# Performance work log

Measured on AMD Instinct MI355X. Metric: run time of the kernel, lower is better.

Reference implementation:

```python
import jax, jax.numpy as jnp
import numpy as np

EMBED_DIM = 512
PATCH = 16
QUANT_N = 1024
QUANT_DIM = 256
LN_EPS = 1e-5


def setup_inputs() -> dict:
    key = jax.random.key(0)
    k1, k2, k3, k4 = jax.random.split(key, 4)
    B, T, M = 16, 8192, 128
    fbank = jax.random.normal(k1, (B, T, M), dtype=jnp.float32)
    # xavier-normal conv weight (O,I,kH,kW), frozen in the original module
    fan = PATCH * PATCH + EMBED_DIM
    conv_w = jax.random.normal(k2, (EMBED_DIM, 1, PATCH, PATCH), dtype=jnp.float32) * np.sqrt(2.0 / fan)
    proj = jax.random.normal(k3, (EMBED_DIM, QUANT_DIM), dtype=jnp.float32) * np.sqrt(2.0 / (EMBED_DIM + QUANT_DIM))
    codebook = jax.random.normal(k4, (QUANT_N, QUANT_DIM), dtype=jnp.float32)
    return {"fbank": fbank, "conv_w": conv_w, "proj": proj, "codebook": codebook}


def _l2norm(x, eps=1e-12):
    return x / jnp.maximum(jnp.linalg.norm(x, axis=-1, keepdims=True), eps)


def reference(fbank, conv_w, proj, codebook):
    # patch embedding: Conv2d(1, D, k=16, s=16) over (B, 1, T, mel)
    x = fbank[:, None, :, :]  # B,1,T,M
    feats = jax.lax.conv_general_dilated(
        x, conv_w, window_strides=(PATCH, PATCH), padding='VALID',
        dimension_numbers=('NCHW', 'OIHW', 'NCHW'))  # B,D,T/16,M/16
    B, D, H, W = feats.shape
    feats = feats.reshape(B, D, H * W).transpose(0, 2, 1)  # B,N,D
    # LayerNorm without affine
    mu = jnp.mean(feats, axis=-1, keepdims=True)
    var = jnp.var(feats, axis=-1, keepdims=True)
    feats = (feats - mu) * jax.lax.rsqrt(var + LN_EPS)
    # random projection quantizer: l2norm(x @ P) vs l2-normalized codebook;
    # argmin euclidean distance == argmax cosine similarity for unit vectors
    p = _l2norm(jnp.einsum('bnd,dq->bnq', feats, proj))  # B,N,Q
    cb = _l2norm(codebook)                                # K,Q
    sim = jnp.einsum('bnq,kq->bnk', p, cb)                # B,N,K
    embed_ind = jnp.argmax(sim, axis=-1)                  # B,N int
    return embed_ind
```

## Files before the change

kernel.cpp:

```cpp
#include <hip/hip_runtime.h>
#include <math.h>

#define QD 256
#define QN 1024
#define TT 8192

typedef __bf16 bf16x8 __attribute__((ext_vector_type(8)));
typedef float  f32x16 __attribute__((ext_vector_type(16)));
typedef unsigned short ushort_t;
typedef unsigned short us8 __attribute__((ext_vector_type(8)));

#define PL  0
#define WS_ 49152
#define P1_ 50176
#define MU_ 51200
#define LM_ 53248
#define TN_ 53376
#define LX_ 54400
#define TH_ 55424
#define CN_ 55552
#define CC_ 55680
#define SMEM_TOTAL 59776

__device__ __forceinline__ void split3(float x, ushort_t& h, ushort_t& m, ushort_t& l) {
    unsigned int xu = __float_as_uint(x);
    h = (ushort_t)(xu >> 16);
    float hf = __uint_as_float(xu & 0xFFFF0000u);
    float r1 = x - hf;
    unsigned int r1u = __float_as_uint(r1);
    m = (ushort_t)(r1u >> 16);
    float mf = __uint_as_float(r1u & 0xFFFF0000u);
    float r2 = r1 - mf;
    l = (ushort_t)(__float_as_uint(r2) >> 16);
}
__device__ __forceinline__ f32x16 MF(bf16x8 a, bf16x8 b, f32x16 c) {
    return __builtin_amdgcn_mfma_f32_32x32x16_bf16(a, b, c, 0, 0, 0);
}

__global__ __launch_bounds__(256) void k_pre(const float* __restrict__ convw,
                                             const float* __restrict__ proj,
                                             const float* __restrict__ cb,
                                             ushort_t* __restrict__ cbph,
                                             float* __restrict__ cbn,
                                             ushort_t* __restrict__ w2p,
                                             float* __restrict__ wsum,
                                             float* __restrict__ p1) {
    int bx = blockIdx.x, t = threadIdx.x;
    if (bx < 256) {
        int c = bx*4 + (t>>6), lane = t&63;
        float4 v = ((const float4*)(cb + (size_t)c*QD))[lane];
        float ss = v.x*v.x + v.y*v.y + v.z*v.z + v.w*v.w;
        #pragma unroll
        for (int off = 32; off > 0; off >>= 1) ss += __shfl_down(ss, off);
        ss = __shfl(ss, 0);
        float inv = 1.0f/fmaxf(sqrtf(ss), 1e-12f);
        float4 vn = make_float4(v.x*inv, v.y*inv, v.z*inv, v.w*inv);
        *(float4*)(cbn + (size_t)c*QD + 4*lane) = vn;
        float vals[4] = {vn.x, vn.y, vn.z, vn.w};
        #pragma unroll
        for (int i = 0; i < 4; ++i) {
            int k = 4*lane + i;
            size_t base = ((size_t)(k>>4)*32 + (c>>5))*512 + (((k>>3)&1)*32 + (c&31))*8 + (k&7);
            cbph[base] = (ushort_t)(__float_as_uint(vals[i]) >> 16);
        }
    } else if (bx < 320) {
        int col0 = (bx - 256) * 4;
        __shared__ float4 colv4[512];
        const float* src = proj + col0;
        colv4[t]       = *(const float4*)(src + (size_t)t * 256);
        colv4[t + 256] = *(const float4*)(src + (size_t)(t + 256) * 256);
        __syncthreads();
        float a0 = 0.f, a1 = 0.f, a2 = 0.f, a3 = 0.f;
        #pragma unroll 16
        for (int d = 0; d < 512; ++d) {
            float wv = convw[d*256 + t];
            float4 cv = colv4[d];
            a0 += wv*cv.x; a1 += wv*cv.y; a2 += wv*cv.z; a3 += wv*cv.w;
        }
        float accs[4] = {a0, a1, a2, a3};
        #pragma unroll
        for (int j = 0; j < 4; ++j) {
            int col = col0 + j;
            ushort_t hb, mb, lb; split3(accs[j], hb, mb, lb);
            size_t base = ((size_t)(t>>4)*8 + (col>>5))*512 + (((t>>3)&1)*32 + (col&31))*8 + (t&7);
            w2p[base] = hb;
            w2p[base + 65536] = mb;
            w2p[base + 131072] = lb;
        }
    } else if (bx == 320) {
        float s = 0.f;
        #pragma unroll 32
        for (int d = 0; d < 512; ++d) s += convw[d*256 + t];
        wsum[t] = s;
    } else {
        float s = 0.f;
        #pragma unroll 32
        for (int d = 0; d < 512; ++d) s += proj[d*256 + t];
        p1[t] = s;
    }
}

__global__ __launch_bounds__(512, 4) void k_mega(const float* __restrict__ fbank,
                                                 const ushort_t* __restrict__ w2p,
                                                 const ushort_t* __restrict__ cbph,
                                                 const float* __restrict__ cbn,
                                                 const float* __restrict__ wsum,
                                                 const float* __restrict__ p1,
                                                 int* __restrict__ out) {
    __shared__ char smem[SMEM_TOTAL];
    float* wsS   = (float*)(smem + WS_);
    float* p1S   = (float*)(smem + P1_);
    float* muS   = (float*)(smem + MU_);
    float* lnMuS = (float*)(smem + LM_);
    float* tn2P  = (float*)(smem + TN_);
    float* lmaxS = (float*)(smem + LX_);
    float* thrS  = (float*)(smem + TH_);
    int*   cntS  = (int*)(smem + CN_);
    ushort_t* candS = (ushort_t*)(smem + CC_);

    int tid = threadIdx.x;
    int n0 = blockIdx.x * 32;
    int w = tid >> 6, lane = tid & 63;
    int n31 = lane & 31, h = lane >> 5;
    size_t loff = (size_t)lane * 16;
    const char* w2pc = (const char*)w2p;
    const char* cbhc = (const char*)cbph;

    auto loadB1 = [&](int kcv, bf16x8 (&dst)[3]) {
        #pragma unroll
        for (int q = 0; q < 3; ++q)
            dst[q] = *(const bf16x8*)(w2pc + (size_t)q*131072 + (size_t)(kcv*8 + w)*1024 + loff);
    };
    auto loadB2 = [&](int kcv, bf16x8 (&dst)[4]) {
        dst[0] = *(const bf16x8*)(cbhc + (size_t)(kcv*32 + w     )*1024 + loff);
        dst[1] = *(const bf16x8*)(cbhc + (size_t)(kcv*32 + w + 8 )*1024 + loff);
        dst[2] = *(const bf16x8*)(cbhc + (size_t)(kcv*32 + w + 16)*1024 + loff);
        dst[3] = *(const bf16x8*)(cbhc + (size_t)(kcv*32 + w + 24)*1024 + loff);
    };
    auto loadA = [&](int kcv, bf16x8 (&a)[3]) {
        #pragma unroll
        for (int p = 0; p < 3; ++p)
            a[p] = *(const bf16x8*)(smem + p*16384 + kcv*1024 + loff);
    };
    auto compute6 = [&](bf16x8 (&a)[3], bf16x8 (&b)[3], f32x16& acc) {
        acc = MF(a[0], b[0], acc);
        acc = MF(a[0], b[1], acc);
        acc = MF(a[1], b[0], acc);
        acc = MF(a[1], b[1], acc);
        acc = MF(a[0], b[2], acc);
        acc = MF(a[2], b[0], acc);
    };

    float4 va[2], vb[2];
    #pragma unroll
    for (int i = 0; i < 2; ++i) {
        int id = tid + 512*i;
        int kc = id >> 6, cl = id & 63;
        int tok = cl & 31, hh2 = cl >> 5;
        int n = n0 + tok;
        int b = n >> 12, r = n & 4095, th = r >> 3, wm = r & 7;
        const float* src = fbank + ((size_t)(b*TT + th*16 + kc))*128 + wm*16 + hh2*8;
        va[i] = ((const float4*)src)[0];
        vb[i] = ((const float4*)src)[1];
    }
    if (tid < 256) wsS[tid] = wsum[tid];
    else           p1S[tid - 256] = p1[tid - 256];
    __syncthreads();

    float mupart = 0.f;
    #pragma unroll
    for (int i = 0; i < 2; ++i) {
        int id = tid + 512*i;
        int kc = id >> 6, cl = id & 63;
        int hh2 = cl >> 5;
        float vals[8] = {va[i].x, va[i].y, va[i].z, va[i].w, vb[i].x, vb[i].y, vb[i].z, vb[i].w};
        us8 hv, mv, lv;
        #pragma unroll
        for (int j = 0; j < 8; ++j) {
            ushort_t a_, b_, c_; split3(vals[j], a_, b_, c_);
            hv[j] = a_; mv[j] = b_; lv[j] = c_;
            mupart += vals[j] * wsS[16*kc + 8*hh2 + j];
        }
        char* cp = smem + kc*1024 + cl*16;
        *(us8*)cp = hv;
        *(us8*)(cp + 16384) = mv;
        *(us8*)(cp + 32768) = lv;
    }

    bf16x8 bA[3], bB[3];
    loadB1(0, bA);

    muS[(tid>>5)*32 + (tid&31)] = mupart;
    __syncthreads();

    if (tid < 32) {
        float pm = 0.f;
        #pragma unroll
        for (int s = 0; s < 16; ++s) pm += muS[s*32 + tid];
        lnMuS[tid] = pm * (1.f/512.f);
    }

    f32x16 accE, accO;
    #pragma unroll
    for (int r2 = 0; r2 < 16; ++r2) { accE[r2] = 0.f; accO[r2] = 0.f; }
    for (int kc = 0; kc < 16; kc += 2) {
        loadB1(kc + 1, bB);
        { bf16x8 a[3]; loadA(kc, a); compute6(a, bA, accE); }
        if (kc + 2 < 16) loadB1(kc + 2, bA);
        { bf16x8 a[3]; loadA(kc + 1, a); compute6(a, bB, accO); }
    }

    bf16x8 qA[4], qB[4];
    loadB2(0, qA);

    __syncthreads();

    {
        int q = 32*w + n31;
        float p1v = p1S[q];
        #pragma unroll
        for (int reg = 0; reg < 16; ++reg) {
            int tok = (reg&3) + 8*(reg>>2) + 4*h;
            float tv = (accE[reg] + accO[reg]) - lnMuS[tok]*p1v;
            *(float*)(smem + 16384 + tok*1024 + q*4) = tv;
            *(ushort_t*)(smem + (q>>4)*1024 + (((q>>3)&1)*32 + tok)*16 + (q&7)*2)
                = (ushort_t)(__float_as_uint(tv) >> 16);
            float sq2 = tv*tv;
            #pragma unroll
            for (int msk = 1; msk < 32; msk <<= 1) sq2 += __shfl_xor(sq2, msk);
            if (n31 == 0) tn2P[tok*8 + w] = sq2;
        }
    }
    __syncthreads();

    f32x16 s0, s1, s2, s3;
    #pragma unroll
    for (int r2 = 0; r2 < 16; ++r2) { s0[r2]=0.f; s1[r2]=0.f; s2[r2]=0.f; s3[r2]=0.f; }
    for (int kc = 0; kc < 16; kc += 2) {
        loadB2(kc + 1, qB);
        {
            bf16x8 ah = *(const bf16x8*)(smem + kc*1024 + loff);
            s0 = MF(ah, qA[0], s0); s1 = MF(ah, qA[1], s1);
            s2 = MF(ah, qA[2], s2); s3 = MF(ah, qA[3], s3);
        }
        if (kc + 2 < 16) loadB2(kc + 2, qA);
        {
            bf16x8 ah = *(const bf16x8*)(smem + (kc+1)*1024 + loff);
            s0 = MF(ah, qB[0], s0); s1 = MF(ah, qB[1], s1);
            s2 = MF(ah, qB[2], s2); s3 = MF(ah, qB[3], s3);
        }
    }
    #pragma unroll
    for (int reg = 0; reg < 16; ++reg) {
        int tok = (reg&3) + 8*(reg>>2) + 4*h;
        float m = fmaxf(fmaxf(s0[reg], s1[reg]), fmaxf(s2[reg], s3[reg]));
        #pragma unroll
        for (int msk = 1; msk < 32; msk <<= 1) m = fmaxf(m, __shfl_xor(m, msk));
        if (n31 == 0) lmaxS[tok*8 + w] = m;
    }
    __syncthreads();
    if (tid < 32) {
        float g = -3.4e38f, sq = 0.f;
        #pragma unroll
        for (int p = 0; p < 8; ++p) { g = fmaxf(g, lmaxS[tid*8 + p]); sq += tn2P[tid*8 + p]; }
        thrS[tid] = g - 0.04f*sqrtf(sq);
        cntS[tid] = 0;
    }
    __syncthreads();
    #pragma unroll
    for (int reg = 0; reg < 16; ++reg) {
        int tok = (reg&3) + 8*(reg>>2) + 4*h;
        float th_ = thrS[tok];
        if (s0[reg] >= th_) { int p = atomicAdd(&cntS[tok], 1); if (p < 64) candS[tok*64 + p] = (ushort_t)(32*(w     ) + n31); }
        if (s1[reg] >= th_) { int p = atomicAdd(&cntS[tok], 1); if (p < 64) candS[tok*64 + p] = (ushort_t)(32*(w + 8 ) + n31); }
        if (s2[reg] >= th_) { int p = atomicAdd(&cntS[tok], 1); if (p < 64) candS[tok*64 + p] = (ushort_t)(32*(w + 16) + n31); }
        if (s3[reg] >= th_) { int p = atomicAdd(&cntS[tok], 1); if (p < 64) candS[tok*64 + p] = (ushort_t)(32*(w + 24) + n31); }
    }
    __syncthreads();
    #pragma unroll 1
    for (int tk = 0; tk < 4; ++tk) {
        int tok = 4*w + tk;
        float4 tv = *(const float4*)(smem + 16384 + tok*1024 + lane*16);
        int nc = cntS[tok];
        bool full = (nc > 64);
        if (full) nc = 1024;
        float bv = -3.4e38f; int bi = 0x7fffffff;
        int c0 = full ? 0 : (int)candS[tok*64];
        float4 v0 = *(const float4*)(cbn + (size_t)c0*256 + 4*lane);
        int c1 = c0; float4 v1 = v0;
        if (nc > 1) {
            c1 = full ? 1 : (int)candS[tok*64 + 1];
            v1 = *(const float4*)(cbn + (size_t)c1*256 + 4*lane);
        }
        for (int c = 0; c < nc; ++c) {
            int c2 = c0; float4 v2 = v0;
            if (c + 2 < nc) {
                c2 = full ? (c + 2) : (int)candS[tok*64 + c + 2];
                v2 = *(const float4*)(cbn + (size_t)c2*256 + 4*lane);
            }
            float d = v0.x*tv.x + v0.y*tv.y + v0.z*tv.z + v0.w*tv.w;
            #pragma unroll
            for (int msk = 1; msk < 64; msk <<= 1) d += __shfl_xor(d, msk);
            if (d > bv || (d == bv && c0 < bi)) { bv = d; bi = c0; }
            c0 = c1; v0 = v1; c1 = c2; v1 = v2;
        }
        if (lane == 0) out[n0 + tok] = bi;
    }
}

extern "C" void kernel_launch(void* const* d_in, const int* in_sizes, int n_in,
                              void* d_out, int out_size, void* d_ws, size_t ws_size,
                              hipStream_t stream) {
    const float* fbank = (const float*)d_in[0];
    const float* convw = (const float*)d_in[1];
    const float* proj  = (const float*)d_in[2];
    const float* cbook = (const float*)d_in[3];
    int* out = (int*)d_out;

    char* ws = (char*)d_ws;
    ushort_t* cbph = (ushort_t*)ws;
    float* cbn     = (float*)(ws + 0x080000);
    ushort_t* w2p  = (ushort_t*)(ws + 0x180000);
    float* wsum    = (float*)(ws + 0x1E0000);
    float* p1      = (float*)(ws + 0x1E1000);

    hipLaunchKernelGGL(k_pre,  dim3(322),  dim3(256), 0, stream,
                       convw, proj, cbook, cbph, cbn, w2p, wsum, p1);
    hipLaunchKernelGGL(k_mega, dim3(2048), dim3(512), 0, stream,
                       fbank, w2p, cbph, cbn, wsum, p1, out);
}
```

Before: 337.0 us.

## Split codebook similarity into two halves and batch candidate rescoring per wave

The bf16 codebook-similarity pass now runs in two sequential halves of 512 codes, each holding two accumulators instead of four. This cuts register pressure, with the running max and threshold updated after each half. Candidate rescoring now scores 16 candidates at once per wave, with 4 lanes per candidate, replacing the one-candidate-per-iteration loop that needed a full 64-lane shuffle reduction. The cost is extra barriers and a threshold that is looser in the first half, which can admit more candidates and make overflow to the full 1024-code scan more likely.

New measurement: 330.1 us. 2.1% less time.

```diff
diff --git a/kernel.cpp b/kernel.cpp
--- a/kernel.cpp
+++ b/kernel.cpp
@@ -131,11 +131,9 @@
         for (int q = 0; q < 3; ++q)
             dst[q] = *(const bf16x8*)(w2pc + (size_t)q*131072 + (size_t)(kcv*8 + w)*1024 + loff);
     };
-    auto loadB2 = [&](int kcv, bf16x8 (&dst)[4]) {
-        dst[0] = *(const bf16x8*)(cbhc + (size_t)(kcv*32 + w     )*1024 + loff);
-        dst[1] = *(const bf16x8*)(cbhc + (size_t)(kcv*32 + w + 8 )*1024 + loff);
-        dst[2] = *(const bf16x8*)(cbhc + (size_t)(kcv*32 + w + 16)*1024 + loff);
-        dst[3] = *(const bf16x8*)(cbhc + (size_t)(kcv*32 + w + 24)*1024 + loff);
+    auto loadB2s = [&](int sw, int kcv, bf16x8 (&dst)[2]) {
+        dst[0] = *(const bf16x8*)(cbhc + (size_t)(kcv*32 + 16*sw + w    )*1024 + loff);
+        dst[1] = *(const bf16x8*)(cbhc + (size_t)(kcv*32 + 16*sw + w + 8)*1024 + loff);
     };
     auto loadA = [&](int kcv, bf16x8 (&a)[3]) {
         #pragma unroll
@@ -210,8 +208,8 @@
         { bf16x8 a[3]; loadA(kc + 1, a); compute6(a, bB, accO); }
     }
 
-    bf16x8 qA[4], qB[4];
-    loadB2(0, qA);
+    bf16x8 qA[2], qB[2];
+    loadB2s(0, 0, qA);
 
     __syncthreads();
 
@@ -233,76 +231,91 @@
     }
     __syncthreads();
 
-    f32x16 s0, s1, s2, s3;
     #pragma unroll
-    for (int r2 = 0; r2 < 16; ++r2) { s0[r2]=0.f; s1[r2]=0.f; s2[r2]=0.f; s3[r2]=0.f; }
-    for (int kc = 0; kc < 16; kc += 2) {
-        loadB2(kc + 1, qB);
-        {
-            bf16x8 ah = *(const bf16x8*)(smem + kc*1024 + loff);
-            s0 = MF(ah, qA[0], s0); s1 = MF(ah, qA[1], s1);
-            s2 = MF(ah, qA[2], s2); s3 = MF(ah, qA[3], s3);
-        }
-        if (kc + 2 < 16) loadB2(kc + 2, qA);
-        {
-            bf16x8 ah = *(const bf16x8*)(smem + (kc+1)*1024 + loff);
-            s0 = MF(ah, qB[0], s0); s1 = MF(ah, qB[1], s1);
-            s2 = MF(ah, qB[2], s2); s3 = MF(ah, qB[3], s3);
-        }
-    }
-    #pragma unroll
-    for (int reg = 0; reg < 16; ++reg) {
-        int tok = (reg&3) + 8*(reg>>2) + 4*h;
-        float m = fmaxf(fmaxf(s0[reg], s1[reg]), fmaxf(s2[reg], s3[reg]));
-        #pragma unroll
-        for (int msk = 1; msk < 32; msk <<= 1) m = fmaxf(m, __shfl_xor(m, msk));
-        if (n31 == 0) lmaxS[tok*8 + w] = m;
-    }
-    __syncthreads();
-    if (tid < 32) {
-        float g = -3.4e38f, sq = 0.f;
-        #pragma unroll
-        for (int p = 0; p < 8; ++p) { g = fmaxf(g, lmaxS[tid*8 + p]); sq += tn2P[tid*8 + p]; }
-        thrS[tid] = g - 0.04f*sqrtf(sq);
-        cntS[tid] = 0;
-    }
-    __syncthreads();
-    #pragma unroll
-    for (int reg = 0; reg < 16; ++reg) {
-        int tok = (reg&3) + 8*(reg>>2) + 4*h;
-        float th_ = thrS[tok];
-        if (s0[reg] >= th_) { int p = atomicAdd(&cntS[tok], 1); if (p < 64) candS[tok*64 + p] = (ushort_t)(32*(w     ) + n31); }
-        if (s1[reg] >= th_) { int p = atomicAdd(&cntS[tok], 1); if (p < 64) candS[tok*64 + p] = (ushort_t)(32*(w + 8 ) + n31); }
-        if (s2[reg] >= th_) { int p = atomicAdd(&cntS[tok], 1); if (p < 64) candS[tok*64 + p] = (ushort_t)(32*(w + 16) + n31); }
-        if (s3[reg] >= th_) { int p = atomicAdd(&cntS[tok], 1); if (p < 64) candS[tok*64 + p] = (ushort_t)(32*(w + 24) + n31); }
-    }
-    __syncthreads();
+    for (int sw = 0; sw < 2; ++sw) {
+        f32x16 s0, s1;
+        #pragma unroll
+        for (int r2 = 0; r2 < 16; ++r2) { s0[r2] = 0.f; s1[r2] = 0.f; }
+        for (int kc = 0; kc < 16; kc += 2) {
+            loadB2s(sw, kc + 1, qB);
+            {
+                bf16x8 ah = *(const bf16x8*)(smem + kc*1024 + loff);
+                s0 = MF(ah, qA[0], s0); s1 = MF(ah, qA[1], s1);
+            }
+            if (kc + 2 < 16) loadB2s(sw, kc + 2, qA);
+            else if (sw == 0) loadB2s(1, 0, qA);
+            {
+                bf16x8 ah = *(const bf16x8*)(smem + (kc+1)*1024 + loff);
+                s0 = MF(ah, qB[0], s0); s1 = MF(ah, qB[1], s1);
+            }
+        }
+        #pragma unroll
+        for (int reg = 0; reg < 16; ++reg) {
+            int tok = (reg&3) + 8*(reg>>2) + 4*h;
+            float m = fmaxf(s0[reg], s1[reg]);
+            #pragma unroll
+            for (int msk = 1; msk < 32; msk <<= 1) m = fmaxf(m, __shfl_xor(m, msk));
+            if (n31 == 0) lmaxS[tok*8 + w] = (sw == 0) ? m : fmaxf(lmaxS[tok*8 + w], m);
+        }
+        __syncthreads();
+        if (tid < 32) {
+            float g = -3.4e38f, sq = 0.f;
+            #pragma unroll
+            for (int p = 0; p < 8; ++p) { g = fmaxf(g, lmaxS[tid*8 + p]); sq += tn2P[tid*8 + p]; }
+            thrS[tid] = g - 0.04f*sqrtf(sq);
+            if (sw == 0) cntS[tid] = 0;
+        }
+        __syncthreads();
+        #pragma unroll
+        for (int reg = 0; reg < 16; ++reg) {
+            int tok = (reg&3) + 8*(reg>>2) + 4*h;
+            float th_ = thrS[tok];
+            if (s0[reg] >= th_) { int p = atomicAdd(&cntS[tok], 1); if (p < 64) candS[tok*64 + p] = (ushort_t)(512*sw + 32*w + n31); }
+            if (s1[reg] >= th_) { int p = atomicAdd(&cntS[tok], 1); if (p < 64) candS[tok*64 + p] = (ushort_t)(512*sw + 32*(w + 8) + n31); }
+        }
+    }
+    __syncthreads();
+
+    int grp = lane >> 2, sub = lane & 3;
     #pragma unroll 1
     for (int tk = 0; tk < 4; ++tk) {
         int tok = 4*w + tk;
-        float4 tv = *(const float4*)(smem + 16384 + tok*1024 + lane*16);
-        int nc = cntS[tok];
-        bool full = (nc > 64);
-        if (full) nc = 1024;
+        int cnt = cntS[tok];
+        bool full = (cnt > 64);
+        int nc = full ? 1024 : cnt;
+        const float4* tp = (const float4*)(smem + 16384 + (size_t)tok*1024 + (size_t)sub*256);
         float bv = -3.4e38f; int bi = 0x7fffffff;
-        int c0 = full ? 0 : (int)candS[tok*64];
-        float4 v0 = *(const float4*)(cbn + (size_t)c0*256 + 4*lane);
-        int c1 = c0; float4 v1 = v0;
-        if (nc > 1) {
-            c1 = full ? 1 : (int)candS[tok*64 + 1];
-            v1 = *(const float4*)(cbn + (size_t)c1*256 + 4*lane);
-        }
-        for (int c = 0; c < nc; ++c) {
-            int c2 = c0; float4 v2 = v0;
-            if (c + 2 < nc) {
-                c2 = full ? (c + 2) : (int)candS[tok*64 + c + 2];
-                v2 = *(const float4*)(cbn + (size_t)c2*256 + 4*lane);
+        #pragma unroll 1
+        for (int base = 0; base < nc; base += 16) {
+            int ci = base + grp;
+            int code = 0x7fffffff;
+            float part = 0.f;
+            if (ci < nc) {
+                code = full ? ci : (int)candS[tok*64 + ci];
+                const float4* cp = (const float4*)(cbn + (size_t)code*256 + (size_t)sub*64);
+                float a0 = 0.f, a1 = 0.f, a2 = 0.f, a3 = 0.f;
+                #pragma unroll
+                for (int j = 0; j < 16; j += 4) {
+                    float4 c0 = cp[j], c1 = cp[j+1], c2 = cp[j+2], c3 = cp[j+3];
+                    float4 t0 = tp[j], t1 = tp[j+1], t2 = tp[j+2], t3 = tp[j+3];
+                    a0 += c0.x*t0.x + c0.y*t0.y + c0.z*t0.z + c0.w*t0.w;
+                    a1 += c1.x*t1.x + c1.y*t1.y + c1.z*t1.z + c1.w*t1.w;
+                    a2 += c2.x*t2.x + c2.y*t2.y + c2.z*t2.z + c2.w*t2.w;
+                    a3 += c3.x*t3.x + c3.y*t3.y + c3.z*t3.z + c3.w*t3.w;
+                }
+                part = (a0 + a1) + (a2 + a3);
             }
-            float d = v0.x*tv.x + v0.y*tv.y + v0.z*tv.z + v0.w*tv.w;
+            float d = part;
+            d += __shfl_xor(d, 1);
+            d += __shfl_xor(d, 2);
+            if (ci >= nc) d = -3.4e38f;
             #pragma unroll
-            for (int msk = 1; msk < 64; msk <<= 1) d += __shfl_xor(d, msk);
-            if (d > bv || (d == bv && c0 < bi)) { bv = d; bi = c0; }
-            c0 = c1; v0 = v1; c1 = c2; v1 = v2;
+            for (int msk = 4; msk < 64; msk <<= 1) {
+                float od = __shfl_xor(d, msk);
+                int   oc = __shfl_xor(code, msk);
+                if (od > d || (od == d && oc < code)) { d = od; code = oc; }
+            }
+            if (d > bv || (d == bv && code < bi)) { bv = d; bi = code; }
         }
         if (lane == 0) out[n0 + tok] = bi;
     }
```
